# Kernel tuning notes

Hardware: AMD Instinct MI355X
Metric: run time of the kernel (lower is better)

The kernel has to match this reference:

```python
import jax, jax.numpy as jnp
import numpy as np

TEMPERATURE = 2.5  # TopKRouter temperature from MoELayer.__init__
TOPK = 2


def setup_inputs() -> dict:
    key = jax.random.key(0)
    ks = jax.random.split(key, 4)
    B, T, D, F, E = 8, 8192, 512, 2048, 8
    x = jax.random.normal(ks[0], (B, T, D), jnp.float32)
    Wr = jax.random.normal(ks[1], (D, E), jnp.float32) * (D ** -0.5)
    W1 = jax.random.normal(ks[2], (E, D, F), jnp.float32) * (D ** -0.5)
    b1 = jnp.zeros((E, F), jnp.float32)
    W2 = jax.random.normal(ks[3], (E, F, D), jnp.float32) * (F ** -0.5)
    b2 = jnp.zeros((E, D), jnp.float32)
    return {"x": x, "Wr": Wr, "W1": W1, "b1": b1, "W2": W2, "b2": b2}


def reference(x, Wr, W1, b1, W2, b2):
    # x: (B, T, D); eval-mode MoE: no router noise, no capacity, no dropout.
    B, T, D = x.shape
    E = Wr.shape[1]
    N = B * T
    xf = x.reshape(N, D)

    # Router: softmax(logits / temperature), then top-k, renormalize kept probs.
    logits = xf @ Wr                                  # (N, E)
    probs = jax.nn.softmax(logits / TEMPERATURE, axis=-1)
    topk_vals, topk_idx = jax.lax.top_k(probs, TOPK)  # (N, K)
    topk_vals = topk_vals / jnp.sum(topk_vals, axis=-1, keepdims=True)

    # Scatter top-k weights into per-expert combine weights w: (N, E).
    w = jnp.zeros((N, E), xf.dtype)
    w = w.at[jnp.arange(N)[:, None], topk_idx].add(topk_vals)

    # Weighted combine of expert FFN outputs (fixed small loop over E experts).
    out = jnp.zeros_like(xf)
    for e in range(E):
        h = jax.nn.gelu(xf @ W1[e] + b1[e])           # (N, F)
        out = out + w[:, e:e + 1] * (h @ W2[e] + b2[e])
    return out.reshape(B, T, D)
```

## Files before the change

### kernel.cpp

```cpp
#include <hip/hip_runtime.h>
#include <cstdint>
#include <cstddef>

#define N_TOK 65536
#define DIM 512
#define FF 2048
#define NE 8
#define HCAP 24576
#define MAXT 1032

typedef __attribute__((ext_vector_type(8))) short short8;
typedef __attribute__((ext_vector_type(4))) float f32x4;

__device__ __forceinline__ unsigned f2bf(float f) {
  unsigned u = __builtin_bit_cast(unsigned, f);
  u = u + 0x7fffu + ((u >> 16) & 1u);
  return (u >> 16) & 0xffffu;
}

__device__ __forceinline__ void gload_lds16(const void* g, void* l) {
  __builtin_amdgcn_global_load_lds((const __attribute__((address_space(1))) void*)g,
                                   (__attribute__((address_space(3))) void*)l, 16, 0, 0);
}

__global__ __launch_bounds__(256) void k_transpose_cast(
    const float* __restrict__ in, unsigned short* __restrict__ outp, int rows, int cols)
{
  __shared__ float tile[32][33];
  const float* ine = in + (size_t)blockIdx.z * rows * cols;
  unsigned short* oute = outp + (size_t)blockIdx.z * rows * cols;
  int tx = threadIdx.x & 31, ty = threadIdx.x >> 5;
  int r0 = blockIdx.y * 32, c0 = blockIdx.x * 32;
#pragma unroll
  for (int i = 0; i < 4; ++i)
    tile[ty + i*8][tx] = ine[(size_t)(r0 + ty + i*8)*cols + c0 + tx];
  __syncthreads();
#pragma unroll
  for (int i = 0; i < 4; ++i) {
    int r = c0 + ty + i*8, c = r0 + tx;
    oute[(size_t)r*rows + c] = (unsigned short)f2bf(tile[tx][ty + i*8]);
  }
}

__global__ __launch_bounds__(256) void k_router(
    const float* __restrict__ x, const float* __restrict__ Wr,
    unsigned short* __restrict__ xb, int2* __restrict__ tinfo, int* __restrict__ cnt)
{
  __shared__ int lcnt[8];
  int tid = threadIdx.x, lane = tid & 63, wv = tid >> 6;
  if (tid < 8) lcnt[tid] = 0;
  float wr[8][8];
#pragma unroll
  for (int j = 0; j < 8; ++j) {
    const float4* p = (const float4*)(Wr + (size_t)(lane*8 + j)*NE);
    float4 a = p[0], b = p[1];
    wr[j][0]=a.x; wr[j][1]=a.y; wr[j][2]=a.z; wr[j][3]=a.w;
    wr[j][4]=b.x; wr[j][5]=b.y; wr[j][6]=b.z; wr[j][7]=b.w;
  }
  __syncthreads();
  int t0 = blockIdx.x*64 + wv*16;
  for (int it = 0; it < 16; ++it) {
    int t = t0 + it;
    const float4* xp = (const float4*)(x + (size_t)t*DIM + lane*8);
    float4 v0 = xp[0], v1 = xp[1];
    float xv[8] = {v0.x,v0.y,v0.z,v0.w,v1.x,v1.y,v1.z,v1.w};
    uint4 pk;
    pk.x = f2bf(xv[0]) | (f2bf(xv[1]) << 16);
    pk.y = f2bf(xv[2]) | (f2bf(xv[3]) << 16);
    pk.z = f2bf(xv[4]) | (f2bf(xv[5]) << 16);
    pk.w = f2bf(xv[6]) | (f2bf(xv[7]) << 16);
    *(uint4*)(xb + (size_t)t*DIM + lane*8) = pk;
    float lg[8];
#pragma unroll
    for (int e2 = 0; e2 < 8; ++e2) lg[e2] = 0.f;
#pragma unroll
    for (int j = 0; j < 8; ++j)
#pragma unroll
      for (int e2 = 0; e2 < 8; ++e2) lg[e2] += xv[j]*wr[j][e2];
#pragma unroll
    for (int off = 32; off >= 1; off >>= 1)
#pragma unroll
      for (int e2 = 0; e2 < 8; ++e2) lg[e2] += __shfl_xor(lg[e2], off, 64);
    int e0 = 0; float v0m = lg[0];
#pragma unroll
    for (int e2 = 1; e2 < 8; ++e2) if (lg[e2] > v0m) { v0m = lg[e2]; e0 = e2; }
    int e1 = -1; float v1m = -3.0e38f;
#pragma unroll
    for (int e2 = 0; e2 < 8; ++e2) if (e2 != e0 && lg[e2] > v1m) { v1m = lg[e2]; e1 = e2; }
    float w0 = 1.f / (1.f + __expf((v1m - v0m) * 0.4f));
    if (lane == 0) {
      atomicAdd(&lcnt[e0], 1);
      atomicAdd(&lcnt[e1], 1);
      tinfo[t] = make_int2(e0 | (e1 << 8), __float_as_int(w0));
    }
  }
  __syncthreads();
  if (tid < 8) atomicAdd(&cnt[tid*16], lcnt[tid]);
}

__global__ void k_offsets(int* cnt) {
  if (threadIdx.x == 0) {
    int base = 0, tb = 0;
    for (int e2 = 0; e2 < 8; ++e2) {
      int c = cnt[e2*16]; if (c > HCAP) c = HCAP;
      cnt[e2*16 + 1] = base;
      base += cnt[e2*16];
      cnt[e2*16 + 2] = 0;
      cnt[e2*16 + 3] = tb;
      tb += (c + 127) >> 7;
    }
    cnt[135] = tb;
  }
}

__global__ __launch_bounds__(128) void k_fill(
    const int2* __restrict__ tinfo, int* __restrict__ tokl,
    float* __restrict__ pwl, int* __restrict__ cnt)
{
  __shared__ int lc[8], lbase[8], gb[8];
  __shared__ unsigned char ce[128];
  __shared__ int csl[128];
  __shared__ float cw[128];
  int tid = threadIdx.x;
  if (tid < 8) { lc[tid] = 0; gb[tid] = cnt[tid*16 + 1]; }
  __syncthreads();
  if (tid < 64) {
    int t = blockIdx.x*64 + tid;
    int2 inf = tinfo[t];
    int e0 = inf.x & 0xff, e1 = (inf.x >> 8) & 0xff;
    float w0 = __int_as_float(inf.y);
    int i0 = tid*2, i1 = i0 + 1;
    ce[i0] = (unsigned char)e0; cw[i0] = w0;        csl[i0] = atomicAdd(&lc[e0], 1);
    ce[i1] = (unsigned char)e1; cw[i1] = 1.f - w0;  csl[i1] = atomicAdd(&lc[e1], 1);
  }
  __syncthreads();
  if (tid < 8) lbase[tid] = atomicAdd(&cnt[tid*16 + 2], lc[tid]);
  __syncthreads();
  int e = ce[tid];
  int p = gb[e] + lbase[e] + csl[tid];
  tokl[p] = blockIdx.x*64 + (tid >> 1);
  pwl[p]  = cw[tid];
}

__device__ __forceinline__ void stage32(
    const unsigned short* __restrict__ src, size_t stride, int k0,
    unsigned short* __restrict__ buf, int tid)
{
#pragma unroll
  for (int j = 0; j < 2; ++j) {
    int lrow = j*64 + (tid >> 2);
    gload_lds16(src + (size_t)lrow*stride + k0 + ((((tid & 3) ^ ((tid >> 3) & 3))) << 3),
                buf + j*2048 + tid*8);
  }
}

__device__ __forceinline__ int tile_expert(const int* cnt, int gt) {
  int e = 0;
#pragma unroll
  for (int k = 1; k < 8; ++k) if (gt >= cnt[k*16 + 3]) e = k;
  return e;
}

__device__ __forceinline__ void mfma_step32(
    const unsigned short* __restrict__ ab, const unsigned short* __restrict__ bb,
    f32x4 acc[4][4], int r16, int g4, int wm, int wn)
{
  short8 af[4], bf[4];
#pragma unroll
  for (int mf = 0; mf < 4; ++mf) {
    int row = wm*64 + mf*16 + r16;
    af[mf] = *(const short8*)(ab + row*32 + ((g4 ^ ((row >> 1) & 3)) << 3));
  }
#pragma unroll
  for (int nf = 0; nf < 4; ++nf) {
    int row = wn*64 + nf*16 + r16;
    bf[nf] = *(const short8*)(bb + row*32 + ((g4 ^ ((row >> 1) & 3)) << 3));
  }
  __builtin_amdgcn_s_setprio(1);
#pragma unroll
  for (int mf = 0; mf < 4; ++mf)
#pragma unroll
    for (int nf = 0; nf < 4; ++nf)
      acc[mf][nf] = __builtin_amdgcn_mfma_f32_16x16x32_bf16(
          af[mf], bf[nf], acc[mf][nf], 0, 0, 0);
  __builtin_amdgcn_s_setprio(0);
}

__global__ __launch_bounds__(256, 4) void k_gemm1(
    const unsigned short* __restrict__ xb, const unsigned short* __restrict__ w1t,
    const float* __restrict__ b1, const int* __restrict__ cnt,
    const int* __restrict__ tokl, unsigned short* __restrict__ h, int T0, int cap)
{
  const int bid = blockIdx.x;
  const int n  = (bid & 7) | (((bid >> 3) & 1) << 3);
  const int lt = bid >> 4;
  const int gt = T0 + lt;
  if (lt >= cap || gt >= cnt[135]) return;
  const int e = tile_expert(cnt, gt);
  const int m = gt - cnt[e*16 + 3];
  const int count0 = cnt[e*16];
  const int count = count0 < HCAP ? count0 : HCAP;
  const int row0 = m*128;
  const int gbase = cnt[e*16 + 1];

  __shared__ __align__(16) unsigned short lds[17408];
  unsigned short* As = lds;
  unsigned short* Bs = lds + 8192;

  const int tid = threadIdx.x, lane = tid & 63, wv = tid >> 6;
  const int r16 = lane & 15, g4 = lane >> 4;
  const int wm = wv >> 1, wn = wv & 1;

  int rows2[2];
#pragma unroll
  for (int j = 0; j < 2; ++j) {
    int rr = row0 + j*64 + (tid >> 2);
    if (rr > count - 1) rr = count - 1;
    rows2[j] = tokl[gbase + rr];
  }
  const int axor = (((tid & 3) ^ ((tid >> 3) & 3))) << 3;
  const unsigned short* w1p = w1t + (size_t)e*FF*DIM + (size_t)(n*128)*DIM;

  auto stageA = [&](unsigned short* buf, int k0) {
#pragma unroll
    for (int j = 0; j < 2; ++j)
      gload_lds16(xb + (size_t)rows2[j]*DIM + k0 + axor, buf + j*2048 + tid*8);
  };

  const f32x4 fz = {0.f, 0.f, 0.f, 0.f};
  f32x4 acc[4][4];
#pragma unroll
  for (int a = 0; a < 4; ++a)
#pragma unroll
    for (int b = 0; b < 4; ++b) acc[a][b] = fz;

  stageA(As, 0);
  stage32(w1p, DIM, 0, Bs, tid);
  __syncthreads();
  int buf = 0;
  for (int kk = 0; kk < DIM/32; ++kk) {
    if (kk + 1 < DIM/32) {
      stageA(As + (buf ^ 1)*4096, (kk + 1)*32);
      stage32(w1p, DIM, (kk + 1)*32, Bs + (buf ^ 1)*4096, tid);
    }
    mfma_step32(As + buf*4096, Bs + buf*4096, acc, r16, g4, wm, wn);
    __syncthreads();
    buf ^= 1;
  }

  float b1v[4];
#pragma unroll
  for (int nf = 0; nf < 4; ++nf)
    b1v[nf] = b1[(size_t)e*FF + n*128 + wn*64 + nf*16 + r16];

  unsigned short* hs = lds;
#pragma unroll
  for (int mf = 0; mf < 4; ++mf)
#pragma unroll
    for (int nf = 0; nf < 4; ++nf) {
      int col = wn*64 + nf*16 + r16;
#pragma unroll
      for (int i = 0; i < 4; ++i) {
        int row = wm*64 + mf*16 + g4*4 + i;
        float v = acc[mf][nf][i] + b1v[nf];
        float u = v * (0.7978845608028654f + 0.0356774081f*v*v);
        float gl = v * __builtin_amdgcn_rcpf(1.f + __expf(-2.f*u));
        hs[row*136 + col] = (unsigned short)f2bf(gl);
      }
    }
  __syncthreads();
  unsigned short* hdst = h + (size_t)lt*(128*FF);
#pragma unroll
  for (int j = 0; j < 8; ++j) {
    int o = j*256 + tid;
    int row = o >> 4, part = o & 15;
    if (row0 + row < count)
      *(uint4*)(hdst + (size_t)row*FF + n*128 + part*8) =
          *(const uint4*)(hs + row*136 + part*8);
  }
}

__global__ __launch_bounds__(256, 4) void k_gemm2(
    const unsigned short* __restrict__ h, const unsigned short* __restrict__ w2t,
    const float* __restrict__ b2, const int* __restrict__ tokl,
    const float* __restrict__ pwl, const int* __restrict__ cnt,
    float* __restrict__ out, int T0, int cap)
{
  const int bid = blockIdx.x;
  const int lt = (bid >> 5)*8 + (bid & 7);
  const int n  = (bid >> 3) & 3;
  const int gt = T0 + lt;
  if (lt >= cap || gt >= cnt[135]) return;
  const int e = tile_expert(cnt, gt);
  const int m = gt - cnt[e*16 + 3];
  const int count0 = cnt[e*16];
  const int count = count0 < HCAP ? count0 : HCAP;
  const int row0 = m*128;
  const int gbase = cnt[e*16 + 1];

  __shared__ __align__(16) unsigned short lds[16384];
  unsigned short* As = lds;
  unsigned short* Bs = lds + 8192;

  const int tid = threadIdx.x, lane = tid & 63, wv = tid >> 6;
  const int r16 = lane & 15, g4 = lane >> 4;
  const int wm = wv >> 1, wn = wv & 1;

  const unsigned short* ap = h + (size_t)lt*(128*FF);
  const unsigned short* bp = w2t + (size_t)e*DIM*FF + (size_t)(n*128)*FF;

  const f32x4 fz = {0.f, 0.f, 0.f, 0.f};
  f32x4 acc[4][4];
#pragma unroll
  for (int a = 0; a < 4; ++a)
#pragma unroll
    for (int b = 0; b < 4; ++b) acc[a][b] = fz;

  stage32(ap, FF, 0, As, tid);
  stage32(bp, FF, 0, Bs, tid);
  __syncthreads();
  int buf = 0;
  for (int kk = 0; kk < FF/32; ++kk) {
    if (kk + 1 < FF/32) {
      stage32(ap, FF, (kk + 1)*32, As + (buf ^ 1)*4096, tid);
      stage32(bp, FF, (kk + 1)*32, Bs + (buf ^ 1)*4096, tid);
    }
    mfma_step32(As + buf*4096, Bs + buf*4096, acc, r16, g4, wm, wn);
    __syncthreads();
    buf ^= 1;
  }

  float b2v[4];
#pragma unroll
  for (int nf = 0; nf < 4; ++nf)
    b2v[nf] = b2[(size_t)e*DIM + n*128 + wn*64 + nf*16 + r16];

#pragma unroll
  for (int mf = 0; mf < 4; ++mf)
#pragma unroll
    for (int i = 0; i < 4; ++i) {
      int lrow = row0 + wm*64 + mf*16 + g4*4 + i;
      if (lrow < count) {
        int tk = tokl[gbase + lrow];
        float wg = pwl[gbase + lrow];
#pragma unroll
        for (int nf = 0; nf < 4; ++nf) {
          int d = n*128 + wn*64 + nf*16 + r16;
          atomicAdd(out + (size_t)tk*DIM + d, (acc[mf][nf][i] + b2v[nf]) * wg);
        }
      }
    }
}

extern "C" void kernel_launch(void* const* d_in, const int* in_sizes, int n_in,
                              void* d_out, int out_size, void* d_ws, size_t ws_size,
                              hipStream_t stream)
{
  const float* x  = (const float*)d_in[0];
  const float* Wr = (const float*)d_in[1];
  const float* W1 = (const float*)d_in[2];
  const float* b1 = (const float*)d_in[3];
  const float* W2 = (const float*)d_in[4];
  const float* b2 = (const float*)d_in[5];
  float* out = (float*)d_out;
  (void)in_sizes; (void)n_in;

  char* ws = (char*)d_ws;
  unsigned short* xb  = (unsigned short*)(ws);
  unsigned short* w1t = (unsigned short*)(ws + 67108864);
  unsigned short* w2t = (unsigned short*)(ws + 83886080);
  int2*  tinfo = (int2*)(ws + 100663296);
  int*   tokl  = (int*)(ws + 101187584);
  float* pwl   = (float*)(ws + 101711872);
  int*   cnt   = (int*)(ws + 102236160);
  unsigned short* h = (unsigned short*)(ws + 102237184);

  const size_t FIXED = 102237184ULL;
  const size_t TILEB = (size_t)128 * FF * 2;
  long cap_l = (ws_size > FIXED) ? (long)((ws_size - FIXED) / TILEB) : 0;
  int cap = (int)(cap_l < MAXT ? cap_l : MAXT);
  if (cap > 256) cap = 256;
  if (cap < 8)  cap = 8;
  const int nch = (MAXT + cap - 1) / cap;
  const int ngrp = (cap + 7) / 8;

  hipMemsetAsync(cnt, 0, 256*sizeof(int), stream);
  hipMemsetAsync(d_out, 0, (size_t)out_size*sizeof(float), stream);

  dim3 g1(FF/32, DIM/32, NE);
  k_transpose_cast<<<g1, 256, 0, stream>>>(W1, w1t, DIM, FF);
  dim3 g2(DIM/32, FF/32, NE);
  k_transpose_cast<<<g2, 256, 0, stream>>>(W2, w2t, FF, DIM);

  k_router<<<N_TOK/64, 256, 0, stream>>>(x, Wr, xb, tinfo, cnt);
  k_offsets<<<1, 64, 0, stream>>>(cnt);
  k_fill<<<N_TOK/64, 128, 0, stream>>>(tinfo, tokl, pwl, cnt);

  for (int c = 0; c < nch; ++c) {
    const int T0 = c * cap;
    k_gemm1<<<ngrp*128, 256, 0, stream>>>(xb, w1t, b1, cnt, tokl, h, T0, cap);
    k_gemm2<<<ngrp*32,  256, 0, stream>>>(h, w2t, b2, tokl, pwl, cnt, out, T0, cap);
  }
}
```

Baseline: 1.080 ms.

## Software-pipeline expert GEMM chunks by fusing gemm2 of chunk c-1 with gemm1 of chunk c

```diff
diff --git a/kernel.cpp b/kernel.cpp
--- a/kernel.cpp
+++ b/kernel.cpp
@@ -8,6 +8,8 @@
 #define NE 8
 #define HCAP 24576
 #define MAXT 1032
+#define CAPF 256
+#define HSLOTS 512
 
 typedef __attribute__((ext_vector_type(8))) short short8;
 typedef __attribute__((ext_vector_type(4))) float f32x4;
@@ -186,16 +188,12 @@
   __builtin_amdgcn_s_setprio(0);
 }
 
-__global__ __launch_bounds__(256, 4) void k_gemm1(
+__device__ __forceinline__ void gemm1_body(
     const unsigned short* __restrict__ xb, const unsigned short* __restrict__ w1t,
     const float* __restrict__ b1, const int* __restrict__ cnt,
-    const int* __restrict__ tokl, unsigned short* __restrict__ h, int T0, int cap)
-{
-  const int bid = blockIdx.x;
-  const int n  = (bid & 7) | (((bid >> 3) & 1) << 3);
-  const int lt = bid >> 4;
-  const int gt = T0 + lt;
-  if (lt >= cap || gt >= cnt[135]) return;
+    const int* __restrict__ tokl, unsigned short* __restrict__ hdst,
+    int gt, int n, unsigned short* lds, int tid)
+{
   const int e = tile_expert(cnt, gt);
   const int m = gt - cnt[e*16 + 3];
   const int count0 = cnt[e*16];
@@ -203,11 +201,9 @@
   const int row0 = m*128;
   const int gbase = cnt[e*16 + 1];
 
-  __shared__ __align__(16) unsigned short lds[17408];
   unsigned short* As = lds;
   unsigned short* Bs = lds + 8192;
-
-  const int tid = threadIdx.x, lane = tid & 63, wv = tid >> 6;
+  const int lane = tid & 63, wv = tid >> 6;
   const int r16 = lane & 15, g4 = lane >> 4;
   const int wm = wv >> 1, wn = wv & 1;
 
@@ -221,12 +217,6 @@
   const int axor = (((tid & 3) ^ ((tid >> 3) & 3))) << 3;
   const unsigned short* w1p = w1t + (size_t)e*FF*DIM + (size_t)(n*128)*DIM;
 
-  auto stageA = [&](unsigned short* buf, int k0) {
-#pragma unroll
-    for (int j = 0; j < 2; ++j)
-      gload_lds16(xb + (size_t)rows2[j]*DIM + k0 + axor, buf + j*2048 + tid*8);
-  };
-
   const f32x4 fz = {0.f, 0.f, 0.f, 0.f};
   f32x4 acc[4][4];
 #pragma unroll
@@ -234,13 +224,18 @@
 #pragma unroll
     for (int b = 0; b < 4; ++b) acc[a][b] = fz;
 
-  stageA(As, 0);
+#pragma unroll
+  for (int j = 0; j < 2; ++j)
+    gload_lds16(xb + (size_t)rows2[j]*DIM + axor, As + j*2048 + tid*8);
   stage32(w1p, DIM, 0, Bs, tid);
   __syncthreads();
   int buf = 0;
   for (int kk = 0; kk < DIM/32; ++kk) {
     if (kk + 1 < DIM/32) {
-      stageA(As + (buf ^ 1)*4096, (kk + 1)*32);
+#pragma unroll
+      for (int j = 0; j < 2; ++j)
+        gload_lds16(xb + (size_t)rows2[j]*DIM + (kk + 1)*32 + axor,
+                    As + (buf ^ 1)*4096 + j*2048 + tid*8);
       stage32(w1p, DIM, (kk + 1)*32, Bs + (buf ^ 1)*4096, tid);
     }
     mfma_step32(As + buf*4096, Bs + buf*4096, acc, r16, g4, wm, wn);
@@ -269,7 +264,6 @@
       }
     }
   __syncthreads();
-  unsigned short* hdst = h + (size_t)lt*(128*FF);
 #pragma unroll
   for (int j = 0; j < 8; ++j) {
     int o = j*256 + tid;
@@ -280,17 +274,12 @@
   }
 }
 
-__global__ __launch_bounds__(256, 4) void k_gemm2(
-    const unsigned short* __restrict__ h, const unsigned short* __restrict__ w2t,
+__device__ __forceinline__ void gemm2_body(
+    const unsigned short* __restrict__ ap, const unsigned short* __restrict__ w2t,
     const float* __restrict__ b2, const int* __restrict__ tokl,
     const float* __restrict__ pwl, const int* __restrict__ cnt,
-    float* __restrict__ out, int T0, int cap)
-{
-  const int bid = blockIdx.x;
-  const int lt = (bid >> 5)*8 + (bid & 7);
-  const int n  = (bid >> 3) & 3;
-  const int gt = T0 + lt;
-  if (lt >= cap || gt >= cnt[135]) return;
+    float* __restrict__ out, int gt, int n, unsigned short* lds, int tid)
+{
   const int e = tile_expert(cnt, gt);
   const int m = gt - cnt[e*16 + 3];
   const int count0 = cnt[e*16];
@@ -298,15 +287,12 @@
   const int row0 = m*128;
   const int gbase = cnt[e*16 + 1];
 
-  __shared__ __align__(16) unsigned short lds[16384];
   unsigned short* As = lds;
   unsigned short* Bs = lds + 8192;
-
-  const int tid = threadIdx.x, lane = tid & 63, wv = tid >> 6;
+  const int lane = tid & 63, wv = tid >> 6;
   const int r16 = lane & 15, g4 = lane >> 4;
   const int wm = wv >> 1, wn = wv & 1;
 
-  const unsigned short* ap = h + (size_t)lt*(128*FF);
   const unsigned short* bp = w2t + (size_t)e*DIM*FF + (size_t)(n*128)*FF;
 
   const f32x4 fz = {0.f, 0.f, 0.f, 0.f};
@@ -350,6 +336,63 @@
         }
       }
     }
+}
+
+__global__ __launch_bounds__(256, 4) void k_gemm1(
+    const unsigned short* __restrict__ xb, const unsigned short* __restrict__ w1t,
+    const float* __restrict__ b1, const int* __restrict__ cnt,
+    const int* __restrict__ tokl, unsigned short* __restrict__ h, int T0, int cap)
+{
+  __shared__ __align__(16) unsigned short lds[17408];
+  const int bid = blockIdx.x;
+  const int n  = (bid & 7) | (((bid >> 3) & 1) << 3);
+  const int lt = bid >> 4;
+  const int gt = T0 + lt;
+  if (lt >= cap || gt >= cnt[135]) return;
+  gemm1_body(xb, w1t, b1, cnt, tokl, h + (size_t)lt*(128*FF), gt, n, lds, threadIdx.x);
+}
+
+__global__ __launch_bounds__(256, 4) void k_gemm2(
+    const unsigned short* __restrict__ h, const unsigned short* __restrict__ w2t,
+    const float* __restrict__ b2, const int* __restrict__ tokl,
+    const float* __restrict__ pwl, const int* __restrict__ cnt,
+    float* __restrict__ out, int T0, int cap)
+{
+  __shared__ __align__(16) unsigned short lds[16384];
+  const int bid = blockIdx.x;
+  const int lt = (bid >> 5)*8 + (bid & 7);
+  const int n  = (bid >> 3) & 3;
+  const int gt = T0 + lt;
+  if (lt >= cap || gt >= cnt[135]) return;
+  gemm2_body(h + (size_t)lt*(128*FF), w2t, b2, tokl, pwl, cnt, out, gt, n, lds, threadIdx.x);
+}
+
+__global__ __launch_bounds__(256, 4) void k_step(
+    const unsigned short* __restrict__ xb, const unsigned short* __restrict__ w1t,
+    const unsigned short* __restrict__ w2t, const float* __restrict__ b1,
+    const float* __restrict__ b2, const int* __restrict__ tokl,
+    const float* __restrict__ pwl, const int* __restrict__ cnt,
+    unsigned short* __restrict__ h, float* __restrict__ out,
+    int T0k2, int T0k1, int nb2)
+{
+  __shared__ __align__(16) unsigned short lds[17408];
+  if ((int)blockIdx.x < nb2) {
+    const int bid = blockIdx.x;
+    const int lt = (bid >> 5)*8 + (bid & 7);
+    const int n  = (bid >> 3) & 3;
+    const int gt = T0k2 + lt;
+    if (lt >= CAPF || gt >= cnt[135]) return;
+    gemm2_body(h + (size_t)(gt & (HSLOTS - 1))*(128*FF), w2t, b2, tokl, pwl, cnt,
+               out, gt, n, lds, threadIdx.x);
+  } else {
+    const int bid = blockIdx.x - nb2;
+    const int n  = (bid & 7) | (((bid >> 3) & 1) << 3);
+    const int lt = bid >> 4;
+    const int gt = T0k1 + lt;
+    if (lt >= CAPF || gt >= cnt[135]) return;
+    gemm1_body(xb, w1t, b1, cnt, tokl, h + (size_t)(gt & (HSLOTS - 1))*(128*FF),
+               gt, n, lds, threadIdx.x);
+  }
 }
 
 extern "C" void kernel_launch(void* const* d_in, const int* in_sizes, int n_in,
@@ -377,12 +420,7 @@
 
   const size_t FIXED = 102237184ULL;
   const size_t TILEB = (size_t)128 * FF * 2;
-  long cap_l = (ws_size > FIXED) ? (long)((ws_size - FIXED) / TILEB) : 0;
-  int cap = (int)(cap_l < MAXT ? cap_l : MAXT);
-  if (cap > 256) cap = 256;
-  if (cap < 8)  cap = 8;
-  const int nch = (MAXT + cap - 1) / cap;
-  const int ngrp = (cap + 7) / 8;
+  const int fused = (ws_size >= FIXED + (size_t)HSLOTS * TILEB);
 
   hipMemsetAsync(cnt, 0, 256*sizeof(int), stream);
   hipMemsetAsync(d_out, 0, (size_t)out_size*sizeof(float), stream);
@@ -396,9 +434,25 @@
   k_offsets<<<1, 64, 0, stream>>>(cnt);
   k_fill<<<N_TOK/64, 128, 0, stream>>>(tinfo, tokl, pwl, cnt);
 
-  for (int c = 0; c < nch; ++c) {
-    const int T0 = c * cap;
-    k_gemm1<<<ngrp*128, 256, 0, stream>>>(xb, w1t, b1, cnt, tokl, h, T0, cap);
-    k_gemm2<<<ngrp*32,  256, 0, stream>>>(h, w2t, b2, tokl, pwl, cnt, out, T0, cap);
-  }
-}
+  if (fused) {
+    const int nch = (MAXT + CAPF - 1) / CAPF;
+    for (int c = 0; c <= nch; ++c) {
+      const int nb2 = (c > 0)   ? CAPF*4  : 0;
+      const int nb1 = (c < nch) ? CAPF*16 : 0;
+      k_step<<<nb2 + nb1, 256, 0, stream>>>(xb, w1t, w2t, b1, b2, tokl, pwl, cnt,
+                                            h, out, (c - 1)*CAPF, c*CAPF, nb2);
+    }
+  } else {
+    long cap_l = (ws_size > FIXED) ? (long)((ws_size - FIXED) / TILEB) : 0;
+    int cap = (int)(cap_l < MAXT ? cap_l : MAXT);
+    if (cap > 256) cap = 256;
+    if (cap < 8)  cap = 8;
+    const int nch = (MAXT + cap - 1) / cap;
+    const int ngrp = (cap + 7) / 8;
+    for (int c = 0; c < nch; ++c) {
+      const int T0 = c * cap;
+      k_gemm1<<<ngrp*128, 256, 0, stream>>>(xb, w1t, b1, cnt, tokl, h, T0, cap);
+      k_gemm2<<<ngrp*32,  256, 0, stream>>>(h, w2t, b2, tokl, pwl, cnt, out, T0, cap);
+    }
+  }
+}
```

After: 1.023 ms. -5.2%, faster.
